# Performance work log

Hardware: AMD Instinct MI355X
Metric: run time of the kernel (lower is better)

Reference implementation:

```python
import jax, jax.numpy as jnp
import numpy as np

OUT = 7        # RoIPool output_size
STRIDE = 16    # feature map stride (forward does cat_rois[:,1:] *= 1/16)


def setup_inputs() -> dict:
    key = jax.random.key(0)
    k1, k2, k3 = jax.random.split(key, 3)
    B, C, H, W, N = 2, 256, 50, 50, 128
    features = jax.random.normal(k1, (B, C, H, W), jnp.float32)
    im = jax.random.randint(k2, (N,), 0, B).astype(jnp.float32)
    # image-space coords in [0, 16*(H-1)] so rounded feature coords stay in-bounds
    coords = jax.random.uniform(k3, (N, 4), jnp.float32, 0.0, float(STRIDE * (H - 1)))
    x1 = jnp.minimum(coords[:, 0], coords[:, 2])
    x2 = jnp.maximum(coords[:, 0], coords[:, 2])
    y1 = jnp.minimum(coords[:, 1], coords[:, 3])
    y2 = jnp.maximum(coords[:, 1], coords[:, 3])
    cat_rois = jnp.stack([im, x1, y1, x2, y2], axis=1)
    return {"features": features, "cat_rois": cat_rois}


def _roi_pool(features, cat_rois):
    # cat_rois[:,1:] *= 1/16 ; round ; cast to int (as in the torch module)
    rois = cat_rois.at[:, 1:].multiply(1.0 / STRIDE)
    rois = jnp.round(rois).astype(jnp.int32)
    im = rois[:, 0]
    x1, y1, x2, y2 = rois[:, 1], rois[:, 2], rois[:, 3], rois[:, 4]
    h = y2 - y1 + 1  # slice y1:y2+1 -> height
    w = x2 - x1 + 1
    H, W = features.shape[2], features.shape[3]

    i = jnp.arange(OUT)
    # AdaptiveMaxPool2d bin boundaries: start=floor(i*h/OUT), end=ceil((i+1)*h/OUT)
    ys = (i[None, :] * h[:, None]) // OUT + y1[:, None]                 # [N,OUT]
    ye = ((i[None, :] + 1) * h[:, None] + OUT - 1) // OUT + y1[:, None]
    xs = (i[None, :] * w[:, None]) // OUT + x1[:, None]
    xe = ((i[None, :] + 1) * w[:, None] + OUT - 1) // OUT + x1[:, None]

    r = jnp.arange(H)
    c = jnp.arange(W)
    row_mask = (r[None, None, :] >= ys[:, :, None]) & (r[None, None, :] < ye[:, :, None])  # [N,OUT,H]
    col_mask = (c[None, None, :] >= xs[:, :, None]) & (c[None, None, :] < xe[:, :, None])  # [N,OUT,W]

    feat = features[im]  # gather per-roi image: [N,C,H,W]
    neg = jnp.finfo(features.dtype).min
    # row pooling: small fixed loop over OUT bins; select fuses into reduce-max
    rp = jnp.stack(
        [jnp.max(jnp.where(row_mask[:, i, :][:, None, :, None], feat, neg), axis=2)
         for i in range(OUT)], axis=2)  # [N,C,OUT,W]
    out = jnp.stack(
        [jnp.max(jnp.where(col_mask[:, j, :][:, None, None, :], rp, neg), axis=3)
         for j in range(OUT)], axis=3)  # [N,C,OUT,OUT]
    return out


def reference(features, cat_rois):
    return _roi_pool(features, cat_rois)
```

## Files before the change

### kernel.cpp

```cpp
#include <hip/hip_runtime.h>
#include <float.h>

#define OUTP 7
#define NCH 256
#define FH 50
#define FW 50

__global__ __launch_bounds__(256) void roi_pool_kernel(
    const float* __restrict__ features,
    const float* __restrict__ cat_rois,
    float* __restrict__ out,
    int total)
{
    int idx = blockIdx.x * blockDim.x + threadIdx.x;
    if (idx >= total) return;

    int j = idx % OUTP;
    int t = idx / OUTP;
    int i = t % OUTP;
    t /= OUTP;
    int c = t % NCH;
    int n = t / NCH;

    const float* r5 = cat_rois + n * 5;
    int im = (int)rintf(r5[0]);
    int x1 = (int)rintf(r5[1] * 0.0625f);
    int y1 = (int)rintf(r5[2] * 0.0625f);
    int x2 = (int)rintf(r5[3] * 0.0625f);
    int y2 = (int)rintf(r5[4] * 0.0625f);

    int h = y2 - y1 + 1;
    int w = x2 - x1 + 1;

    int ys = i * h / OUTP + y1;
    int ye = ((i + 1) * h + OUTP - 1) / OUTP + y1;
    int xs = j * w / OUTP + x1;
    int xe = ((j + 1) * w + OUTP - 1) / OUTP + x1;

    ys = max(ys, 0);  ye = min(ye, FH);
    xs = max(xs, 0);  xe = min(xe, FW);

    const float* base = features + ((size_t)(im * NCH + c)) * (FH * FW);

    float m = -FLT_MAX;
    for (int r = ys; r < ye; ++r) {
        const float* row = base + r * FW;
        for (int x = xs; x < xe; ++x) {
            m = fmaxf(m, row[x]);
        }
    }
    out[idx] = m;
}

extern "C" void kernel_launch(void* const* d_in, const int* in_sizes, int n_in,
                              void* d_out, int out_size, void* d_ws, size_t ws_size,
                              hipStream_t stream) {
    const float* features = (const float*)d_in[0];
    const float* cat_rois = (const float*)d_in[1];
    float* out = (float*)d_out;

    int total = out_size;
    int block = 256;
    int grid = (total + block - 1) / block;
    roi_pool_kernel<<<grid, block, 0, stream>>>(features, cat_rois, out, total);
}
```

Before: 82.10 us.

## Stage ROI region in LDS per channel and pool bins from shared memory

The kernel is restructured so each block handles one ROI and four channels. Each wavefront copies the ROI's feature region into LDS with coalesced row loads, then 49 lanes compute the bin maxima from LDS. Before, every output bin read global memory on its own, so overlapping bins and strided per-thread reads were paid again and again. In exchange, ROI coordinates are no longer clamped to the feature map, only lanes below w load, and most lanes sit idle during the reduction.

```diff
diff --git a/kernel.cpp b/kernel.cpp
--- a/kernel.cpp
+++ b/kernel.cpp
@@ -5,51 +5,57 @@
 #define NCH 256
 #define FH 50
 #define FW 50
+#define CPB 4
 
-__global__ __launch_bounds__(256) void roi_pool_kernel(
+__global__ __launch_bounds__(256) void roi_pool_opt(
     const float* __restrict__ features,
     const float* __restrict__ cat_rois,
-    float* __restrict__ out,
-    int total)
+    float* __restrict__ out)
 {
-    int idx = blockIdx.x * blockDim.x + threadIdx.x;
-    if (idx >= total) return;
+    __shared__ float lds[CPB][FH * FW];
 
-    int j = idx % OUTP;
-    int t = idx / OUTP;
-    int i = t % OUTP;
-    t /= OUTP;
-    int c = t % NCH;
-    int n = t / NCH;
+    const int n    = blockIdx.x;
+    const int lane = threadIdx.x & 63;
+    const int quad = threadIdx.x >> 6;
+    const int c    = blockIdx.y * CPB + quad;
 
     const float* r5 = cat_rois + n * 5;
-    int im = (int)rintf(r5[0]);
-    int x1 = (int)rintf(r5[1] * 0.0625f);
-    int y1 = (int)rintf(r5[2] * 0.0625f);
-    int x2 = (int)rintf(r5[3] * 0.0625f);
-    int y2 = (int)rintf(r5[4] * 0.0625f);
+    const int im = (int)rintf(r5[0]);
+    const int x1 = (int)rintf(r5[1] * 0.0625f);
+    const int y1 = (int)rintf(r5[2] * 0.0625f);
+    const int x2 = (int)rintf(r5[3] * 0.0625f);
+    const int y2 = (int)rintf(r5[4] * 0.0625f);
 
-    int h = y2 - y1 + 1;
-    int w = x2 - x1 + 1;
+    const int h = y2 - y1 + 1;
+    const int w = x2 - x1 + 1;
 
-    int ys = i * h / OUTP + y1;
-    int ye = ((i + 1) * h + OUTP - 1) / OUTP + y1;
-    int xs = j * w / OUTP + x1;
-    int xe = ((j + 1) * w + OUTP - 1) / OUTP + x1;
-
-    ys = max(ys, 0);  ye = min(ye, FH);
-    xs = max(xs, 0);  xe = min(xe, FW);
-
-    const float* base = features + ((size_t)(im * NCH + c)) * (FH * FW);
-
-    float m = -FLT_MAX;
-    for (int r = ys; r < ye; ++r) {
-        const float* row = base + r * FW;
-        for (int x = xs; x < xe; ++x) {
-            m = fmaxf(m, row[x]);
+    const float* base = features + ((size_t)(im * NCH + c)) * (FH * FW)
+                                 + y1 * FW + x1;
+    float* ldsq = lds[quad];
+    if (lane < w) {
+        for (int r = 0; r < h; ++r) {
+            ldsq[r * w + lane] = base[r * FW + lane];
         }
     }
-    out[idx] = m;
+    __syncthreads();
+
+    if (lane < OUTP * OUTP) {
+        const int i = lane / OUTP;
+        const int j = lane % OUTP;
+        const int ys = i * h / OUTP;
+        const int ye = ((i + 1) * h + OUTP - 1) / OUTP;
+        const int xs = j * w / OUTP;
+        const int xe = ((j + 1) * w + OUTP - 1) / OUTP;
+
+        float m = -FLT_MAX;
+        for (int r = ys; r < ye; ++r) {
+            const float* row = ldsq + r * w;
+            for (int x = xs; x < xe; ++x) {
+                m = fmaxf(m, row[x]);
+            }
+        }
+        out[(((size_t)n * NCH + c) * OUTP + i) * OUTP + j] = m;
+    }
 }
 
 extern "C" void kernel_launch(void* const* d_in, const int* in_sizes, int n_in,
@@ -59,8 +65,7 @@
     const float* cat_rois = (const float*)d_in[1];
     float* out = (float*)d_out;
 
-    int total = out_size;
-    int block = 256;
-    int grid = (total + block - 1) / block;
-    roi_pool_kernel<<<grid, block, 0, stream>>>(features, cat_rois, out, total);
+    const int N = in_sizes[1] / 5;
+    dim3 grid(N, NCH / CPB);
+    roi_pool_opt<<<grid, 256, 0, stream>>>(features, cat_rois, out);
 }
```

New measurement: 98.63 us. +20.1%, slower.
